# Kernel optimization log

Hardware: AMD Instinct MI355X
Metric: run time of the kernel (lower is better)

## Reference

```python
import jax, jax.numpy as jnp
import numpy as np

N = 33           # n_nodes (fixed by lstm1 input_size = 512*33)
T = 1024         # seq_length
E_RAND = 64      # random directed edges
E = E_RAND + N   # plus self-loops (PyG GATv2Conv add_self_loops=True)
H1, C1 = 8, 64   # gat1: heads, out_channels
C2 = 512         # gat2: out_channels, 1 head
D_IN, D_EDGE = 2, 3
HID1, HID2, N_CLASSES = 128, 64, 4


def _p(k, shape):
    return jax.random.normal(k, shape, dtype=jnp.float32) * 0.05


def setup_inputs() -> dict:
    key = jax.random.key(0)
    ks = jax.random.split(key, 30)
    src = jax.random.randint(ks[0], (E_RAND,), 0, N)
    dst = jax.random.randint(ks[1], (E_RAND,), 0, N)
    loop = jnp.arange(N)
    edge_index = jnp.stack([jnp.concatenate([src, loop]),
                            jnp.concatenate([dst, loop])]).astype(jnp.int32)
    return {
        'x': jax.random.normal(ks[2], (T, N, D_IN), dtype=jnp.float32),
        'edge_index': edge_index,
        'edge_attr': jax.random.normal(ks[3], (E, D_EDGE), dtype=jnp.float32),
        'g1_wl': _p(ks[4], (D_IN, H1 * C1)),
        'g1_wr': _p(ks[5], (D_IN, H1 * C1)),
        'g1_we': _p(ks[6], (D_EDGE, H1 * C1)),
        'g1_att': _p(ks[7], (H1, C1)),
        'g1_b': _p(ks[8], (H1 * C1,)),
        'g2_wl': _p(ks[9], (H1 * C1, C2)),
        'g2_wr': _p(ks[10], (H1 * C1, C2)),
        'g2_we': _p(ks[11], (D_EDGE, C2)),
        'g2_att': _p(ks[12], (1, C2)),
        'g2_b': _p(ks[13], (C2,)),
        'l1_wih': _p(ks[14], (4 * HID1, N * C2)),
        'l1_whh': _p(ks[15], (4 * HID1, HID1)),
        'l1_bih': _p(ks[16], (4 * HID1,)),
        'l1_bhh': _p(ks[17], (4 * HID1,)),
        'l2_wih': _p(ks[18], (4 * HID2, HID1)),
        'l2_whh': _p(ks[19], (4 * HID2, HID2)),
        'l2_bih': _p(ks[20], (4 * HID2,)),
        'l2_bhh': _p(ks[21], (4 * HID2,)),
        'fc_w': _p(ks[22], (N_CLASSES, HID2)),
        'fc_b': _p(ks[23], (N_CLASSES,)),
    }


def _gatv2(x, src, dst, edge_attr, wl, wr, we, att, bias, heads, ch):
    # GATv2 with edge features, vectorized over the time axis.
    # x: [T,N,Din] -> out [T,N,heads*ch]
    Tt, Nn, _ = x.shape
    xl = (x @ wl).reshape(Tt, Nn, heads, ch)   # source projection
    xr = (x @ wr).reshape(Tt, Nn, heads, ch)   # target projection
    ep = (edge_attr @ we).reshape(-1, heads, ch)
    msg = xl[:, src]                                        # [T,E,H,C]
    e = jax.nn.leaky_relu(msg + xr[:, dst] + ep[None], 0.2)  # GATv2 score input
    logits = jnp.einsum('tehc,hc->eth', e, att)             # edge-first [E,T,H]
    m = jax.ops.segment_max(logits, dst, num_segments=Nn)
    m = jnp.where(jnp.isneginf(m), 0.0, m)
    ex = jnp.exp(logits - m[dst])
    denom = jax.ops.segment_sum(ex, dst, num_segments=Nn)
    alpha = ex / (denom[dst] + 1e-16)                       # [E,T,H]
    out = jax.ops.segment_sum(alpha[..., None] * jnp.swapaxes(msg, 0, 1),
                              dst, num_segments=Nn)          # [N,T,H,C]
    return jnp.swapaxes(out, 0, 1).reshape(Tt, Nn, heads * ch) + bias


def _lstm(xs, wih, whh, bih, bhh):
    # PyTorch LSTM, batch=1, gate order i,f,g,o. xs: [T,D] -> [T,H]
    hd = whh.shape[1]
    def step(carry, xt):
        h, c = carry
        z = xt @ wih.T + h @ whh.T + bih + bhh
        i, f, g, o = jnp.split(z, 4)
        c = jax.nn.sigmoid(f) * c + jax.nn.sigmoid(i) * jnp.tanh(g)
        h = jax.nn.sigmoid(o) * jnp.tanh(c)
        return (h, c), h
    h0 = jnp.zeros((hd,), xs.dtype)
    _, hs = jax.lax.scan(step, (h0, h0), xs)
    return hs


def _forward(edge_index, x, edge_attr, g1_wl, g1_wr, g1_we, g1_att, g1_b,
             g2_wl, g2_wr, g2_we, g2_att, g2_b,
             l1_wih, l1_whh, l1_bih, l1_bhh,
             l2_wih, l2_whh, l2_bih, l2_bhh, fc_w, fc_b):
    src, dst = edge_index[0], edge_index[1]
    h = jax.nn.elu(_gatv2(x, src, dst, edge_attr, g1_wl, g1_wr, g1_we, g1_att, g1_b, H1, C1))
    h = jax.nn.elu(_gatv2(h, src, dst, edge_attr, g2_wl, g2_wr, g2_we, g2_att, g2_b, 1, C2))
    # torch: stack [T,N,512] -> permute(1,0,2) -> reshape(1, T, N*512)
    seq = jnp.transpose(h, (1, 0, 2)).reshape(T, N * C2)
    hs = _lstm(seq, l1_wih, l1_whh, l1_bih, l1_bhh)
    hs = _lstm(hs, l2_wih, l2_whh, l2_bih, l2_bhh)
    return (hs[-1] @ fc_w.T + fc_b)[None, :]  # [1, n_classes]


def reference(x, edge_index, edge_attr, g1_wl, g1_wr, g1_we, g1_att, g1_b,
              g2_wl, g2_wr, g2_we, g2_att, g2_b,
              l1_wih, l1_whh, l1_bih, l1_bhh,
              l2_wih, l2_whh, l2_bih, l2_bhh, fc_w, fc_b):
    return _forward(edge_index, x, edge_attr, g1_wl, g1_wr, g1_we, g1_att, g1_b,
                    g2_wl, g2_wr, g2_we, g2_att, g2_b,
                    l1_wih, l1_whh, l1_bih, l1_bhh,
                    l2_wih, l2_whh, l2_bih, l2_bhh, fc_w, fc_b)
```

## Files before the change

kernel.cpp:

```cpp
#include <hip/hip_runtime.h>

typedef unsigned short u16;
typedef unsigned int   u32;
typedef __attribute__((ext_vector_type(8))) short  short8;
typedef __attribute__((ext_vector_type(8))) unsigned short ushort8;
typedef __attribute__((ext_vector_type(4))) float  f32x4;

#define NT 1024
#define NN 33
#define NE 97

__device__ __forceinline__ float b2f(u16 u){ return __uint_as_float(((u32)u)<<16); }
__device__ __forceinline__ u16 f2b(float f){
    u32 x = __float_as_uint(f);
    return (u16)((x + 0x7fffu + ((x>>16)&1u)) >> 16);
}
__device__ __forceinline__ float sigm(float x){ return 1.f/(1.f+__expf(-x)); }
__device__ __forceinline__ float tanh_(float x){ float e=__expf(2.f*x); return 1.f - 2.f/(e+1.f); }

__global__ void detect_kernel(const u32* g1_wl_raw, int* flag){
    if (threadIdx.x==0 && blockIdx.x==0){
        int hits=0;
        for (int k=0;k<256;k++){
            u32 w = g1_wl_raw[k];
            u32 e = (w>>7)&0xffu;
            if (e>=96u && e<=126u) hits++;
        }
        *flag = (hits>=160) ? 0 : 1;
    }
}

struct ConvArgs { const void* src[22]; int n[22]; int off[22]; };
__global__ void convert_kernel(ConvArgs a, const int* flag, u16* blob){
    bool isf32 = (*flag)!=0;
    int stride = gridDim.x*blockDim.x;
    for (int s=0;s<22;s++){
        int n=a.n[s]; const void* sp=a.src[s]; u16* dp=blob+a.off[s];
        for (int i=blockIdx.x*blockDim.x+threadIdx.x; i<n; i+=stride)
            dp[i] = isf32 ? f2b(((const float*)sp)[i]) : ((const u16*)sp)[i];
    }
}

#define CX      0
#define CEA     67584
#define CG1WL   67880
#define CG1WR   68904
#define CG1WE   69928
#define CG1ATT  71464
#define CG1B    71976
#define CG2WL   72488
#define CG2WR   334632
#define CG2WE   596776
#define CG2ATT  598312
#define CG2B    598824
#define CL1WIH  599336
#define CL1WHH  9250088
#define CL1BIH  9315624
#define CL1BHH  9316136
#define CL2WIH  9316648
#define CL2WHH  9349416
#define CL2BIH  9365800
#define CL2BHH  9366056
#define CFCW    9366312
#define CFCB    9366568

__global__ void setup_kernel(const int* ei, const u16* ea,
                             const u16* g1_we, const u16* g2_we,
                             int* csr, float* ep1, float* ep2)
{
    int tid = threadIdx.x;
    if (tid == 0) {
        int cnt[NN]; for (int n=0;n<NN;n++) cnt[n]=0;
        for (int e=0;e<NE;e++) cnt[ei[NE+e]]++;
        int off=0;
        for (int n=0;n<NN;n++){ csr[n]=off; off+=cnt[n]; }
        csr[NN]=off;
        int pos[NN]; for (int n=0;n<NN;n++) pos[n]=csr[n];
        for (int e=0;e<NE;e++){ int d=ei[NE+e]; csr[34+pos[d]]=e; pos[d]++; }
        for (int e=0;e<NE;e++){ csr[131+e]=ei[e]; csr[228+e]=ei[NE+e]; }
    }
    for (int i=tid; i<NE*512; i+=blockDim.x) {
        int e = i>>9, hc = i&511;
        float a0=b2f(ea[e*3]), a1=b2f(ea[e*3+1]), a2=b2f(ea[e*3+2]);
        ep1[i] = a0*b2f(g1_we[hc]) + a1*b2f(g1_we[512+hc]) + a2*b2f(g1_we[1024+hc]);
        ep2[i] = a0*b2f(g2_we[hc]) + a1*b2f(g2_we[512+hc]) + a2*b2f(g2_we[1024+hc]);
    }
}

__global__ void wlrt_kernel(const u16* g2_wl, const u16* g2_wr, u16* wlrt)
{
    int i = blockIdx.x*256 + threadIdx.x;
    int k = i>>9, c = i&511;
    wlrt[c*512 + k]        = g2_wl[i];
    wlrt[(c+512)*512 + k]  = g2_wr[i];
}

__global__ void permw_kernel(const u16* w1hh, const u16* w2ih, const u16* w2hh,
                             u16* w1p, u16* w2ip, u16* w2hp)
{
    int i0 = blockIdx.x*256 + threadIdx.x;
    int stride = gridDim.x*256;
    for (int j=i0; j<65536; j+=stride){
        int r=j>>7, k=j&127, u=r>>2, g=r&3;
        w1p[j] = w1hh[(g*128+u)*128 + k];
    }
    for (int j=i0; j<32768; j+=stride){
        int r=j>>7, k=j&127, u=r>>2, g=r&3;
        w2ip[j] = w2ih[(g*64+u)*128 + k];
    }
    for (int j=i0; j<16384; j+=stride){
        int r=j>>6, k=j&63, u=r>>2, g=r&3;
        w2hp[j] = w2hh[(g*64+u)*64 + k];
    }
}

__global__ __launch_bounds__(256) void gat1_kernel(
    const u16* x, const u16* g1_wl, const u16* g1_wr, const u16* g1_att,
    const u16* g1_b, const float* ep1, const int* csr, u16* h1)
{
    __shared__ float wl[2][512], wr[2][512], att[512], bias[512];
    __shared__ float xt[2*NN];
    __shared__ float logits[NE*8];
    __shared__ float mmax[NN*8], den[NN*8];
    __shared__ int s_off[NN+1], s_eid[NE], s_src[NE], s_dst[NE];
    int t = blockIdx.x, tid = threadIdx.x;

    for (int i=tid;i<512;i+=256){
        wl[0][i]=b2f(g1_wl[i]);      wl[1][i]=b2f(g1_wl[512+i]);
        wr[0][i]=b2f(g1_wr[i]);      wr[1][i]=b2f(g1_wr[512+i]);
        att[i]=b2f(g1_att[i]);       bias[i]=b2f(g1_b[i]);
    }
    for (int i=tid;i<2*NN;i+=256) xt[i]=b2f(x[t*(2*NN)+i]);
    if (tid<NN+1) s_off[tid]=csr[tid];
    for (int i=tid;i<NE;i+=256){ s_eid[i]=csr[34+i]; s_src[i]=csr[131+i]; s_dst[i]=csr[228+i]; }
    __syncthreads();

    for (int i=tid; i<NE*8; i+=256) {
        int e=i>>3, h=i&7;
        int s=s_src[e], d=s_dst[e];
        float xs0=xt[s*2], xs1=xt[s*2+1], xd0=xt[d*2], xd1=xt[d*2+1];
        const float* epp = ep1 + e*512 + h*64;
        float acc=0.f;
        #pragma unroll 8
        for (int c=0;c<64;c++){
            int hc=h*64+c;
            float v = xs0*wl[0][hc] + xs1*wl[1][hc]
                    + xd0*wr[0][hc] + xd1*wr[1][hc] + epp[c];
            v = v>0.f ? v : 0.2f*v;
            acc += att[hc]*v;
        }
        logits[i]=acc;
    }
    __syncthreads();
    for (int i=tid; i<NN*8; i+=256) {
        int n=i>>3, h=i&7;
        float m=-1e30f;
        for (int p=s_off[n]; p<s_off[n+1]; ++p){ float v=logits[s_eid[p]*8+h]; m=v>m?v:m; }
        float s=0.f;
        for (int p=s_off[n]; p<s_off[n+1]; ++p) s += __expf(logits[s_eid[p]*8+h]-m);
        mmax[i]=m; den[i]=s+1e-16f;
    }
    __syncthreads();
    for (int i=tid; i<NE*8; i+=256) {
        int h=i&7, d=s_dst[i>>3];
        logits[i] = __expf(logits[i]-mmax[d*8+h]) / den[d*8+h];
    }
    __syncthreads();
    for (int i=tid; i<NN*512; i+=256) {
        int n=i>>9, hc=i&511, h=hc>>6;
        float acc=0.f;
        for (int p=s_off[n]; p<s_off[n+1]; ++p){
            int e=s_eid[p]; int s=s_src[e];
            float xlv = xt[s*2]*wl[0][hc] + xt[s*2+1]*wl[1][hc];
            acc += logits[e*8+h]*xlv;
        }
        acc += bias[hc];
        acc = acc>0.f ? acc : __expf(acc)-1.f;
        h1[(size_t)(t*NN+n)*512 + hc] = f2b(acc);
    }
}

__global__ __launch_bounds__(256) void gemm_nt(
    const u16* __restrict__ A, const u16* __restrict__ B, void* Cout,
    int M, int N, int K, int kChunk, int mode)
{
    __shared__ u16 lds_a[128*40];
    __shared__ u16 lds_b[128*40];
    const int nt = blockIdx.x, mt = blockIdx.y, kc = blockIdx.z;
    const int tid = threadIdx.x;
    const int wave = tid>>6, lane = tid&63;
    const int wm = (wave&1)*64, wn = (wave>>1)*64;
    const int l15 = lane&15, quad = lane>>4;
    const int srow = tid>>2, scol = (tid&3)*8;

    const u16* Ab = A + (size_t)mt*128*K;
    const u16* Bb = B + (size_t)nt*128*K;
    const int k0beg = kc*kChunk, k0end = k0beg + kChunk;

    f32x4 acc[4][4] = {};
    for (int k0 = k0beg; k0 < k0end; k0 += 32) {
        #pragma unroll
        for (int r = 0; r < 2; ++r) {
            int row = srow + r*64;
            *(ushort8*)&lds_a[row*40 + scol] = *(const ushort8*)&Ab[(size_t)row*K + k0 + scol];
            *(ushort8*)&lds_b[row*40 + scol] = *(const ushort8*)&Bb[(size_t)row*K + k0 + scol];
        }
        __syncthreads();
        short8 af[4], bfr[4];
        #pragma unroll
        for (int i=0;i<4;i++) af[i]  = *(const short8*)&lds_a[(wm + i*16 + l15)*40 + quad*8];
        #pragma unroll
        for (int j=0;j<4;j++) bfr[j] = *(const short8*)&lds_b[(wn + j*16 + l15)*40 + quad*8];
        #pragma unroll
        for (int i=0;i<4;i++)
            #pragma unroll
            for (int j=0;j<4;j++)
                acc[i][j] = __builtin_amdgcn_mfma_f32_16x16x32_bf16(af[i], bfr[j], acc[i][j], 0,0,0);
        __syncthreads();
    }
    if (mode == 0) {
        u16* Cb = (u16*)Cout;
        #pragma unroll
        for (int i=0;i<4;i++)
            #pragma unroll
            for (int j=0;j<4;j++)
                #pragma unroll
                for (int r=0;r<4;r++){
                    int row = mt*128 + wm + i*16 + quad*4 + r;
                    int col = nt*128 + wn + j*16 + l15;
                    Cb[(size_t)row*N + col] = f2b(acc[i][j][r]);
                }
    } else {
        float* Cb = (float*)Cout + (size_t)kc*M*N;
        #pragma unroll
        for (int i=0;i<4;i++)
            #pragma unroll
            for (int j=0;j<4;j++)
                #pragma unroll
                for (int r=0;r<4;r++){
                    int row = mt*128 + wm + i*16 + quad*4 + r;
                    int col = nt*128 + wn + j*16 + l15;
                    Cb[(size_t)row*N + col] = acc[i][j][r];
                }
    }
}

__global__ void reduce8_kernel(const float* part, float* out)
{
    int i = blockIdx.x*256 + threadIdx.x;
    float s=0.f;
    #pragma unroll
    for (int k=0;k<8;k++) s += part[(size_t)k*524288 + i];
    int t=i>>9, c=i&511;
    out[t*512 + ((c&127)<<2) + (c>>7)] = s;
}

__global__ __launch_bounds__(256) void gat2_kernel(
    const u16* C, const u16* g2_att, const u16* g2_b, const float* ep2,
    const int* csr, u16* h2)
{
    __shared__ u16 xl[NN*512];
    __shared__ float att[512], bias[512];
    __shared__ float part[NE*8];
    __shared__ float logit[NE], alpha[NE], mm[NN], dd[NN];
    __shared__ int s_off[NN+1], s_eid[NE], s_src[NE], s_dst[NE];
    int t = blockIdx.x, tid = threadIdx.x;

    for (int i=tid;i<512;i+=256){ att[i]=b2f(g2_att[i]); bias[i]=b2f(g2_b[i]); }
    if (tid<NN+1) s_off[tid]=csr[tid];
    for (int i=tid;i<NE;i+=256){ s_eid[i]=csr[34+i]; s_src[i]=csr[131+i]; s_dst[i]=csr[228+i]; }
    for (int i=tid; i<NN*64; i+=256){
        int n=i>>6, q=i&63;
        *(ushort8*)&xl[n*512+q*8] = *(const ushort8*)&C[(size_t)(t*NN+n)*1024 + q*8];
    }
    __syncthreads();

    for (int i=tid; i<NE*8; i+=256){
        int e=i>>3, q=i&7;
        int s=s_src[e], d=s_dst[e];
        const u16* xrp = C + (size_t)(t*NN+d)*1024 + 512 + q*64;
        const float* epp = ep2 + e*512 + q*64;
        const u16* xlp = xl + s*512 + q*64;
        float acc=0.f;
        #pragma unroll 8
        for (int c=0;c<64;c++){
            float v = b2f(xlp[c]) + b2f(xrp[c]) + epp[c];
            v = v>0.f ? v : 0.2f*v;
            acc += att[q*64+c]*v;
        }
        part[i]=acc;
    }
    __syncthreads();
    for (int i=tid;i<NE;i+=256){
        float s=0.f;
        #pragma unroll
        for (int q=0;q<8;q++) s+=part[i*8+q];
        logit[i]=s;
    }
    __syncthreads();
    for (int i=tid;i<NN;i+=256){
        float m=-1e30f;
        for (int p=s_off[i];p<s_off[i+1];++p){ float v=logit[s_eid[p]]; m=v>m?v:m; }
        float s=0.f;
        for (int p=s_off[i];p<s_off[i+1];++p) s+=__expf(logit[s_eid[p]]-m);
        mm[i]=m; dd[i]=s+1e-16f;
    }
    __syncthreads();
    for (int i=tid;i<NE;i+=256) alpha[i]=__expf(logit[i]-mm[s_dst[i]])/dd[s_dst[i]];
    __syncthreads();
    for (int i=tid;i<NN*512;i+=256){
        int n=i>>9, c=i&511;
        float acc=0.f;
        for (int p=s_off[n];p<s_off[n+1];++p){ int e=s_eid[p]; acc += alpha[e]*b2f(xl[s_src[e]*512+c]); }
        acc += bias[c];
        acc = acc>0.f ? acc : __expf(acc)-1.f;
        h2[(size_t)n*524288 + (size_t)t*512 + c] = f2b(acc);
    }
}

__global__ __launch_bounds__(512) void lstm_fused_kernel(
    const float* __restrict__ pre1p,
    const u16* __restrict__ w1p, const u16* b1ih, const u16* b1hh,
    const u16* __restrict__ w2ip, const u16* __restrict__ w2hp,
    const u16* b2ih, const u16* b2hh,
    const u16* fc_w, const u16* fc_b, const int* flag, void* outv)
{
    __shared__ __align__(16) float pre_c[32*512];
    __shared__ __align__(16) u16 hb1[2][128];
    __shared__ __align__(16) u16 hb2[2][64];
    __shared__ float hf[64];
    const int tid = threadIdx.x;
    const int wave = tid>>6, lane = tid&63;
    const int l15 = lane&15, quad = lane>>4;
    const f32x4 fz = {0.f,0.f,0.f,0.f};
    const float4* p4g = (const float4*)pre1p;
    float4* c4 = (float4*)pre_c;

    if (tid<128) hb1[1][tid]=0;
    if (tid<64)  hb2[1][tid]=0;

    if (wave < 4) {
        short8 af[8][4];
        #pragma unroll
        for (int i=0;i<8;i++)
            #pragma unroll
            for (int c=0;c<4;c++)
                af[i][c] = *(const short8*)&w1p[(size_t)(wave*128 + i*16 + l15)*128 + c*32 + quad*8];
        const int u = wave*32 + ((l15<8)?l15:0)*4 + quad;
        const float bz0 = b2f(b1ih[u])     + b2f(b1hh[u]);
        const float bz1 = b2f(b1ih[128+u]) + b2f(b1hh[128+u]);
        const float bz2 = b2f(b1ih[256+u]) + b2f(b1hh[256+u]);
        const float bz3 = b2f(b1ih[384+u]) + b2f(b1hh[384+u]);
        float c1 = 0.f;
        __syncthreads();
        for (int k=0;k<1025;k++){
            if (k<1024 && (k&31)==0){
                #pragma unroll
                for (int j=0;j<8;j++) c4[j*512+tid] = p4g[(size_t)k*128 + j*512 + tid];
                __syncthreads();
            }
            if (k<1024){
                float4 pf = {0.f,0.f,0.f,0.f};
                if (l15<8) pf = *(const float4*)&pre_c[(k&31)*512 + wave*128 + l15*16 + quad*4];
                const u16* hp = hb1[(k+1)&1];
                short8 b0 = *(const short8*)&hp[quad*8];
                short8 b1 = *(const short8*)&hp[32+quad*8];
                short8 b2 = *(const short8*)&hp[64+quad*8];
                short8 b3 = *(const short8*)&hp[96+quad*8];
                f32x4 acc[8];
                #pragma unroll
                for (int i=0;i<8;i++){
                    f32x4 a = __builtin_amdgcn_mfma_f32_16x16x32_bf16(af[i][0], b0, fz, 0,0,0);
                    a = __builtin_amdgcn_mfma_f32_16x16x32_bf16(af[i][1], b1, a, 0,0,0);
                    a = __builtin_amdgcn_mfma_f32_16x16x32_bf16(af[i][2], b2, a, 0,0,0);
                    a = __builtin_amdgcn_mfma_f32_16x16x32_bf16(af[i][3], b3, a, 0,0,0);
                    acc[i] = a;
                }
                f32x4 z = acc[0];
                #pragma unroll
                for (int i=1;i<8;i++) z = (l15==i) ? acc[i] : z;
                if (l15<8){
                    float zi = z[0]+pf.x+bz0;
                    float zf = z[1]+pf.y+bz1;
                    float zg = z[2]+pf.z+bz2;
                    float zo = z[3]+pf.w+bz3;
                    c1 = sigm(zf)*c1 + sigm(zi)*tanh_(zg);
                    float ho = sigm(zo)*tanh_(c1);
                    hb1[k&1][u] = f2b(ho);
                }
            }
            __syncthreads();
        }
    } else {
        const int wv = wave-4;
        short8 af[4][6];
        #pragma unroll
        for (int i=0;i<4;i++){
            int r = wv*64 + i*16 + l15;
            #pragma unroll
            for (int c=0;c<4;c++)
                af[i][c] = *(const short8*)&w2ip[(size_t)r*128 + c*32 + quad*8];
            #pragma unroll
            for (int c=0;c<2;c++)
                af[i][4+c] = *(const short8*)&w2hp[(size_t)r*64 + c*32 + quad*8];
        }
        const int u2 = wv*16 + ((l15<4)?l15:0)*4 + quad;
        const float bz0 = b2f(b2ih[u2])     + b2f(b2hh[u2]);
        const float bz1 = b2f(b2ih[64+u2])  + b2f(b2hh[64+u2]);
        const float bz2 = b2f(b2ih[128+u2]) + b2f(b2hh[128+u2]);
        const float bz3 = b2f(b2ih[192+u2]) + b2f(b2hh[192+u2]);
        float c2s = 0.f;
        __syncthreads();
        for (int k=0;k<1025;k++){
            if (k<1024 && (k&31)==0){
                #pragma unroll
                for (int j=0;j<8;j++) c4[j*512+tid] = p4g[(size_t)k*128 + j*512 + tid];
                __syncthreads();
            }
            if (k>=1){
                const u16* hp1 = hb1[(k-1)&1];
                const u16* hp2 = hb2[k&1];
                short8 b0 = *(const short8*)&hp1[quad*8];
                short8 b1 = *(const short8*)&hp1[32+quad*8];
                short8 b2 = *(const short8*)&hp1[64+quad*8];
                short8 b3 = *(const short8*)&hp1[96+quad*8];
                short8 b4 = *(const short8*)&hp2[quad*8];
                short8 b5 = *(const short8*)&hp2[32+quad*8];
                f32x4 acc[4];
                #pragma unroll
                for (int i=0;i<4;i++){
                    f32x4 a = __builtin_amdgcn_mfma_f32_16x16x32_bf16(af[i][0], b0, fz, 0,0,0);
                    a = __builtin_amdgcn_mfma_f32_16x16x32_bf16(af[i][1], b1, a, 0,0,0);
                    a = __builtin_amdgcn_mfma_f32_16x16x32_bf16(af[i][2], b2, a, 0,0,0);
                    a = __builtin_amdgcn_mfma_f32_16x16x32_bf16(af[i][3], b3, a, 0,0,0);
                    a = __builtin_amdgcn_mfma_f32_16x16x32_bf16(af[i][4], b4, a, 0,0,0);
                    a = __builtin_amdgcn_mfma_f32_16x16x32_bf16(af[i][5], b5, a, 0,0,0);
                    acc[i] = a;
                }
                f32x4 z = acc[0];
                #pragma unroll
                for (int i=1;i<4;i++) z = (l15==i) ? acc[i] : z;
                if (l15<4){
                    float zi = z[0]+bz0;
                    float zf = z[1]+bz1;
                    float zg = z[2]+bz2;
                    float zo = z[3]+bz3;
                    c2s = sigm(zf)*c2s + sigm(zi)*tanh_(zg);
                    float ho = sigm(zo)*tanh_(c2s);
                    hb2[(k-1)&1][u2] = f2b(ho);
                    hf[u2] = ho;
                }
            }
            __syncthreads();
        }
    }
    __syncthreads();
    if (tid<4){
        float acc = b2f(fc_b[tid]);
        #pragma unroll
        for (int j=0;j<64;j++) acc += hf[j]*b2f(fc_w[tid*64+j]);
        if (*flag) ((float*)outv)[tid] = acc;
        else       ((u16*)outv)[tid]  = f2b(acc);
    }
}

extern "C" void kernel_launch(void* const* d_in, const int* in_sizes, int n_in,
                              void* d_out, int out_size, void* d_ws, size_t ws_size,
                              hipStream_t stream) {
    const int* ei = (const int*)d_in[1];
    char* ws = (char*)d_ws;

    const size_t o_blob = 0;
    const size_t o_h    = 18733184;
    const size_t o_C    = o_h    + 34603008;
    const size_t o_wlrt = o_C    + 69206016;
    const size_t o_ep1  = o_wlrt + 1048576;
    const size_t o_ep2  = o_ep1  + 198656;
    const size_t o_csr  = o_ep2  + 198656;
    const size_t o_pre1 = o_csr  + 2048;
    const size_t o_w1p  = o_pre1 + 2097152;
    const size_t o_w2ip = o_w1p  + 131072;
    const size_t o_w2hp = o_w2ip + 65536;

    u16*   blob  = (u16*)(ws + o_blob);
    u16*   h_buf = (u16*)(ws + o_h);
    u16*   Cbuf  = (u16*)(ws + o_C);
    u16*   wlrt  = (u16*)(ws + o_wlrt);
    float* ep1   = (float*)(ws + o_ep1);
    float* ep2   = (float*)(ws + o_ep2);
    int*   csr   = (int*)(ws + o_csr);
    int*   flag  = csr + 400;
    float* pre1  = (float*)(ws + o_pre1);
    u16*   w1p   = (u16*)(ws + o_w1p);
    u16*   w2ip  = (u16*)(ws + o_w2ip);
    u16*   w2hp  = (u16*)(ws + o_w2hp);
    float* part  = (float*)(ws + o_C);

    detect_kernel<<<1,64,0,stream>>>((const u32*)d_in[3], flag);

    ConvArgs ca;
    const int blob_off[22] = {CX,CEA,CG1WL,CG1WR,CG1WE,CG1ATT,CG1B,
                              CG2WL,CG2WR,CG2WE,CG2ATT,CG2B,
                              CL1WIH,CL1WHH,CL1BIH,CL1BHH,
                              CL2WIH,CL2WHH,CL2BIH,CL2BHH,CFCW,CFCB};
    const int in_idx[22]   = {0,2,3,4,5,6,7,8,9,10,11,12,13,14,15,16,17,18,19,20,21,22};
    for (int s=0;s<22;s++){
        ca.src[s]=d_in[in_idx[s]]; ca.n[s]=in_sizes[in_idx[s]]; ca.off[s]=blob_off[s];
    }
    convert_kernel<<<2048,256,0,stream>>>(ca, flag, blob);

    setup_kernel<<<1,256,0,stream>>>(ei, blob+CEA, blob+CG1WE, blob+CG2WE, csr, ep1, ep2);
    wlrt_kernel<<<1024,256,0,stream>>>(blob+CG2WL, blob+CG2WR, wlrt);
    permw_kernel<<<64,256,0,stream>>>(blob+CL1WHH, blob+CL2WIH, blob+CL2WHH, w1p, w2ip, w2hp);
    gat1_kernel<<<NT,256,0,stream>>>(blob+CX, blob+CG1WL, blob+CG1WR, blob+CG1ATT,
                                     blob+CG1B, ep1, csr, h_buf);
    gemm_nt<<<dim3(8,264,1),256,0,stream>>>(h_buf, wlrt, Cbuf, 33792, 1024, 512, 512, 0);
    gat2_kernel<<<NT,256,0,stream>>>(Cbuf, blob+CG2ATT, blob+CG2B, ep2, csr, h_buf);
    gemm_nt<<<dim3(4,8,8),256,0,stream>>>(h_buf, blob+CL1WIH, part, 1024, 512, 16896, 2112, 1);
    reduce8_kernel<<<2048,256,0,stream>>>(part, pre1);
    lstm_fused_kernel<<<1,512,0,stream>>>(pre1,
        w1p, blob+CL1BIH, blob+CL1BHH,
        w2ip, w2hp, blob+CL2BIH, blob+CL2BHH,
        blob+CFCW, blob+CFCB, flag, d_out);
}
```

Before: 1.502 ms.

## Batch LSTM2 input projection over 16-step chunks and spread both layers across all waves

```diff
diff --git a/kernel.cpp b/kernel.cpp
--- a/kernel.cpp
+++ b/kernel.cpp
@@ -326,6 +326,8 @@
     const u16* fc_w, const u16* fc_b, const int* flag, void* outv)
 {
     __shared__ __align__(16) float pre_c[32*512];
+    __shared__ __align__(16) u16 h1hist[32*136];
+    __shared__ __align__(16) float z2ih[16*264];
     __shared__ __align__(16) u16 hb1[2][128];
     __shared__ __align__(16) u16 hb2[2][64];
     __shared__ float hf[64];
@@ -336,125 +338,123 @@
     const float4* p4g = (const float4*)pre1p;
     float4* c4 = (float4*)pre_c;
 
+    short8 af1[4][4];
+    #pragma unroll
+    for (int i=0;i<4;i++)
+        #pragma unroll
+        for (int c=0;c<4;c++)
+            af1[i][c] = *(const short8*)&w1p[(size_t)(wave*64 + i*16 + l15)*128 + c*32 + quad*8];
+    short8 af2[2][2];
+    #pragma unroll
+    for (int j=0;j<2;j++)
+        #pragma unroll
+        for (int c=0;c<2;c++)
+            af2[j][c] = *(const short8*)&w2hp[(size_t)(wave*32 + j*16 + l15)*64 + c*32 + quad*8];
+    short8 af3[2][4];
+    #pragma unroll
+    for (int j=0;j<2;j++)
+        #pragma unroll
+        for (int c=0;c<4;c++)
+            af3[j][c] = *(const short8*)&w2ip[(size_t)(wave*32 + j*16 + l15)*128 + c*32 + quad*8];
+
+    int uu = 0;
+    float bz0=0,bz1=0,bz2=0,bz3=0;
+    if (l15<4){
+        uu = wave*16 + l15*4 + quad;
+        bz0 = b2f(b1ih[uu])     + b2f(b1hh[uu]);
+        bz1 = b2f(b1ih[128+uu]) + b2f(b1hh[128+uu]);
+        bz2 = b2f(b1ih[256+uu]) + b2f(b1hh[256+uu]);
+        bz3 = b2f(b1ih[384+uu]) + b2f(b1hh[384+uu]);
+    } else if (l15<6){
+        uu = wave*8 + (l15-4)*4 + quad;
+        bz0 = b2f(b2ih[uu])     + b2f(b2hh[uu]);
+        bz1 = b2f(b2ih[64+uu])  + b2f(b2hh[64+uu]);
+        bz2 = b2f(b2ih[128+uu]) + b2f(b2hh[128+uu]);
+        bz3 = b2f(b2ih[192+uu]) + b2f(b2hh[192+uu]);
+    }
+    float cst = 0.f;
+
     if (tid<128) hb1[1][tid]=0;
-    if (tid<64)  hb2[1][tid]=0;
-
-    if (wave < 4) {
-        short8 af[8][4];
-        #pragma unroll
-        for (int i=0;i<8;i++)
+    if (tid<64){ hb2[0][tid]=0; hb2[1][tid]=0; }
+
+    for (int k=0;k<1040;k++){
+        if (k<1024 && (k&31)==0){
+            #pragma unroll
+            for (int j=0;j<8;j++) c4[j*512+tid] = p4g[(size_t)k*128 + j*512 + tid];
+            __syncthreads();
+        }
+        if ((k&15)==0 && k>=16 && k<=1024){
+            int cs = k-16;
+            short8 hbv[4];
             #pragma unroll
             for (int c=0;c<4;c++)
-                af[i][c] = *(const short8*)&w1p[(size_t)(wave*128 + i*16 + l15)*128 + c*32 + quad*8];
-        const int u = wave*32 + ((l15<8)?l15:0)*4 + quad;
-        const float bz0 = b2f(b1ih[u])     + b2f(b1hh[u]);
-        const float bz1 = b2f(b1ih[128+u]) + b2f(b1hh[128+u]);
-        const float bz2 = b2f(b1ih[256+u]) + b2f(b1hh[256+u]);
-        const float bz3 = b2f(b1ih[384+u]) + b2f(b1hh[384+u]);
-        float c1 = 0.f;
+                hbv[c] = *(const short8*)&h1hist[((cs+l15)&31)*136 + c*32 + quad*8];
+            f32x4 bacc0=fz, bacc1=fz;
+            #pragma unroll
+            for (int c=0;c<4;c++){
+                bacc0 = __builtin_amdgcn_mfma_f32_16x16x32_bf16(af3[0][c], hbv[c], bacc0, 0,0,0);
+                bacc1 = __builtin_amdgcn_mfma_f32_16x16x32_bf16(af3[1][c], hbv[c], bacc1, 0,0,0);
+            }
+            *(f32x4*)&z2ih[l15*264 + wave*32 + quad*4]      = bacc0;
+            *(f32x4*)&z2ih[l15*264 + wave*32 + 16 + quad*4] = bacc1;
+            __syncthreads();
+        }
+        const u16* hp1 = hb1[(k+1)&1];
+        const u16* hp2 = hb2[(k+1)&1];
+        short8 b1f[4];
+        #pragma unroll
+        for (int c=0;c<4;c++) b1f[c] = *(const short8*)&hp1[c*32 + quad*8];
+        short8 b2f_[2];
+        #pragma unroll
+        for (int c=0;c<2;c++) b2f_[c] = *(const short8*)&hp2[c*32 + quad*8];
+
+        f32x4 acc1[4] = {fz,fz,fz,fz};
+        if (k<1024){
+            #pragma unroll
+            for (int c=0;c<4;c++)
+                #pragma unroll
+                for (int i=0;i<4;i++)
+                    acc1[i] = __builtin_amdgcn_mfma_f32_16x16x32_bf16(af1[i][c], b1f[c], acc1[i], 0,0,0);
+        }
+        f32x4 acc2[2] = {fz,fz};
+        if (k>=16){
+            #pragma unroll
+            for (int c=0;c<2;c++)
+                #pragma unroll
+                for (int j=0;j<2;j++)
+                    acc2[j] = __builtin_amdgcn_mfma_f32_16x16x32_bf16(af2[j][c], b2f_[c], acc2[j], 0,0,0);
+        }
+        float4 pf = {0.f,0.f,0.f,0.f};
+        if (l15<4){
+            pf = *(const float4*)&pre_c[(k&31)*512 + uu*4];
+        } else if (l15<6 && k>=16){
+            pf = *(const float4*)&z2ih[((k-16)&15)*264 + uu*4];
+        }
+        f32x4 z1s = acc1[0];
+        z1s = (l15==1) ? acc1[1] : z1s;
+        z1s = (l15==2) ? acc1[2] : z1s;
+        z1s = (l15==3) ? acc1[3] : z1s;
+        f32x4 z2s = (l15==5) ? acc2[1] : acc2[0];
+        f32x4 zz  = (l15<4) ? z1s : z2s;
+        bool act = (l15<4) ? (k<1024) : (l15<6 && k>=16);
+        if (act){
+            float zi = zz[0]+pf.x+bz0;
+            float zf = zz[1]+pf.y+bz1;
+            float zg = zz[2]+pf.z+bz2;
+            float zo = zz[3]+pf.w+bz3;
+            cst = sigm(zf)*cst + sigm(zi)*tanh_(zg);
+            float ho = sigm(zo)*tanh_(cst);
+            u16 hv = f2b(ho);
+            if (l15<4){
+                hb1[k&1][uu] = hv;
+                h1hist[(k&31)*136 + uu] = hv;
+            } else {
+                hb2[k&1][uu] = hv;
+                hf[uu] = ho;
+            }
+        }
         __syncthreads();
-        for (int k=0;k<1025;k++){
-            if (k<1024 && (k&31)==0){
-                #pragma unroll
-                for (int j=0;j<8;j++) c4[j*512+tid] = p4g[(size_t)k*128 + j*512 + tid];
-                __syncthreads();
-            }
-            if (k<1024){
-                float4 pf = {0.f,0.f,0.f,0.f};
-                if (l15<8) pf = *(const float4*)&pre_c[(k&31)*512 + wave*128 + l15*16 + quad*4];
-                const u16* hp = hb1[(k+1)&1];
-                short8 b0 = *(const short8*)&hp[quad*8];
-                short8 b1 = *(const short8*)&hp[32+quad*8];
-                short8 b2 = *(const short8*)&hp[64+quad*8];
-                short8 b3 = *(const short8*)&hp[96+quad*8];
-                f32x4 acc[8];
-                #pragma unroll
-                for (int i=0;i<8;i++){
-                    f32x4 a = __builtin_amdgcn_mfma_f32_16x16x32_bf16(af[i][0], b0, fz, 0,0,0);
-                    a = __builtin_amdgcn_mfma_f32_16x16x32_bf16(af[i][1], b1, a, 0,0,0);
-                    a = __builtin_amdgcn_mfma_f32_16x16x32_bf16(af[i][2], b2, a, 0,0,0);
-                    a = __builtin_amdgcn_mfma_f32_16x16x32_bf16(af[i][3], b3, a, 0,0,0);
-                    acc[i] = a;
-                }
-                f32x4 z = acc[0];
-                #pragma unroll
-                for (int i=1;i<8;i++) z = (l15==i) ? acc[i] : z;
-                if (l15<8){
-                    float zi = z[0]+pf.x+bz0;
-                    float zf = z[1]+pf.y+bz1;
-                    float zg = z[2]+pf.z+bz2;
-                    float zo = z[3]+pf.w+bz3;
-                    c1 = sigm(zf)*c1 + sigm(zi)*tanh_(zg);
-                    float ho = sigm(zo)*tanh_(c1);
-                    hb1[k&1][u] = f2b(ho);
-                }
-            }
-            __syncthreads();
-        }
-    } else {
-        const int wv = wave-4;
-        short8 af[4][6];
-        #pragma unroll
-        for (int i=0;i<4;i++){
-            int r = wv*64 + i*16 + l15;
-            #pragma unroll
-            for (int c=0;c<4;c++)
-                af[i][c] = *(const short8*)&w2ip[(size_t)r*128 + c*32 + quad*8];
-            #pragma unroll
-            for (int c=0;c<2;c++)
-                af[i][4+c] = *(const short8*)&w2hp[(size_t)r*64 + c*32 + quad*8];
-        }
-        const int u2 = wv*16 + ((l15<4)?l15:0)*4 + quad;
-        const float bz0 = b2f(b2ih[u2])     + b2f(b2hh[u2]);
-        const float bz1 = b2f(b2ih[64+u2])  + b2f(b2hh[64+u2]);
-        const float bz2 = b2f(b2ih[128+u2]) + b2f(b2hh[128+u2]);
-        const float bz3 = b2f(b2ih[192+u2]) + b2f(b2hh[192+u2]);
-        float c2s = 0.f;
-        __syncthreads();
-        for (int k=0;k<1025;k++){
-            if (k<1024 && (k&31)==0){
-                #pragma unroll
-                for (int j=0;j<8;j++) c4[j*512+tid] = p4g[(size_t)k*128 + j*512 + tid];
-                __syncthreads();
-            }
-            if (k>=1){
-                const u16* hp1 = hb1[(k-1)&1];
-                const u16* hp2 = hb2[k&1];
-                short8 b0 = *(const short8*)&hp1[quad*8];
-                short8 b1 = *(const short8*)&hp1[32+quad*8];
-                short8 b2 = *(const short8*)&hp1[64+quad*8];
-                short8 b3 = *(const short8*)&hp1[96+quad*8];
-                short8 b4 = *(const short8*)&hp2[quad*8];
-                short8 b5 = *(const short8*)&hp2[32+quad*8];
-                f32x4 acc[4];
-                #pragma unroll
-                for (int i=0;i<4;i++){
-                    f32x4 a = __builtin_amdgcn_mfma_f32_16x16x32_bf16(af[i][0], b0, fz, 0,0,0);
-                    a = __builtin_amdgcn_mfma_f32_16x16x32_bf16(af[i][1], b1, a, 0,0,0);
-                    a = __builtin_amdgcn_mfma_f32_16x16x32_bf16(af[i][2], b2, a, 0,0,0);
-                    a = __builtin_amdgcn_mfma_f32_16x16x32_bf16(af[i][3], b3, a, 0,0,0);
-                    a = __builtin_amdgcn_mfma_f32_16x16x32_bf16(af[i][4], b4, a, 0,0,0);
-                    a = __builtin_amdgcn_mfma_f32_16x16x32_bf16(af[i][5], b5, a, 0,0,0);
-                    acc[i] = a;
-                }
-                f32x4 z = acc[0];
-                #pragma unroll
-                for (int i=1;i<4;i++) z = (l15==i) ? acc[i] : z;
-                if (l15<4){
-                    float zi = z[0]+bz0;
-                    float zf = z[1]+bz1;
-                    float zg = z[2]+bz2;
-                    float zo = z[3]+bz3;
-                    c2s = sigm(zf)*c2s + sigm(zi)*tanh_(zg);
-                    float ho = sigm(zo)*tanh_(c2s);
-                    hb2[(k-1)&1][u2] = f2b(ho);
-                    hf[u2] = ho;
-                }
-            }
-            __syncthreads();
-        }
-    }
-    __syncthreads();
+    }
     if (tid<4){
         float acc = b2f(fc_b[tid]);
         #pragma unroll
```

After: 1.635 ms. 1.09x slower.
